# Kernel optimization log

Hardware: AMD Instinct MI355X
Metric: run time of the kernel (lower is better)

## Reference

```python
import jax, jax.numpy as jnp
import numpy as np

B, L, D, NUM_NODES = 256, 512, 128, 1024


def setup_inputs() -> dict:
    key = jax.random.key(0)
    k1, k2, k3, k4, k5, k6 = jax.random.split(key, 6)
    src_ids = jax.random.randint(k1, (B, L), 0, NUM_NODES, dtype=jnp.int32)
    dst_ids = jax.random.randint(k2, (B, L), 0, NUM_NODES, dtype=jnp.int32)
    s = 1.0  # nn.Linear default init is uniform; randn is fine for a numeric baseline
    W1 = jax.random.normal(k3, (1, D), dtype=jnp.float32) * s
    b1 = jax.random.normal(k4, (D,), dtype=jnp.float32) * 0.01
    W2 = jax.random.normal(k5, (D, D), dtype=jnp.float32) * (1.0 / np.sqrt(D))
    b2 = jax.random.normal(k6, (D,), dtype=jnp.float32) * 0.01
    return {"src_ids": src_ids, "dst_ids": dst_ids, "W1": W1, "b1": b1, "W2": W2, "b2": b2}


def _counts_in(a, b):
    # counts_in[i, j] = number of occurrences of a[i, j] within b[i, :]
    # matches np.unique counts / dict-lookup semantics (missing key -> 0)
    return (a[:, :, None] == b[:, None, :]).sum(axis=-1).astype(jnp.float32)


def _encode(appearances, W1, b1, W2, b2):
    # appearances: (B, L, 2) -> unsqueeze(-1) -> Linear(1, D) -> ReLU -> Linear(D, D) -> sum over the 2 count channels
    h = jax.nn.relu(appearances[..., None] * W1[0] + b1)      # (B, L, 2, D)
    h = jnp.einsum('blcd,de->blce', h, W2) + b2               # (B, L, 2, D)
    return h.sum(axis=2)                                      # (B, L, D)


def reference(src_ids, dst_ids, W1, b1, W2, b2):
    # co-occurrence appearance counts
    src_app = jnp.stack([_counts_in(src_ids, src_ids), _counts_in(src_ids, dst_ids)], axis=-1)  # (B, Ls, 2)
    dst_app = jnp.stack([_counts_in(dst_ids, src_ids), _counts_in(dst_ids, dst_ids)], axis=-1)  # (B, Ld, 2)
    # zero out padded positions (node id == 0)
    src_app = jnp.where(src_ids[..., None] == 0, 0.0, src_app)
    dst_app = jnp.where(dst_ids[..., None] == 0, 0.0, dst_app)
    src_feat = _encode(src_app, W1, b1, W2, b2)
    dst_feat = _encode(dst_app, W1, b1, W2, b2)
    return src_feat, dst_feat
```

## Files before the change

kernel.cpp:

```cpp
#include <hip/hip_runtime.h>


#define BB      256
#define LL      512
#define DD      128
#define NNODES  1024
#define CMAX    512
#define SPLITS  4
#define ROWS_PER (LL / SPLITS)

typedef float f4x __attribute__((ext_vector_type(4)));

__global__ __launch_bounds__(DD) void build_table_kernel(
    const float* __restrict__ W1, const float* __restrict__ b1,
    const float* __restrict__ W2, const float* __restrict__ b2,
    float* __restrict__ T) {
  const int c = blockIdx.x;
  const int e = threadIdx.x;
  __shared__ float h[DD];
  h[e] = fmaxf((float)c * W1[e] + b1[e], 0.0f);
  __syncthreads();
  float acc = b2[e];
#pragma unroll 16
  for (int d = 0; d < DD; ++d) acc = fmaf(h[d], W2[d * DD + e], acc);
  T[c * DD + e] = acc;
}

__global__ __launch_bounds__(256) void encode_kernel(
    const int* __restrict__ src_ids, const int* __restrict__ dst_ids,
    const float* __restrict__ T, float* __restrict__ out) {
  const int batch = blockIdx.x >> 2;
  const int split = blockIdx.x & (SPLITS - 1);
  const int tid   = threadIdx.x;

  __shared__ int hist[2 * NNODES];
  __shared__ int cnt[4 * ROWS_PER];

#pragma unroll
  for (int i = tid; i < 2 * NNODES; i += 256) hist[i] = 0;
  __syncthreads();

  const int* sb = src_ids + batch * LL;
  const int* db = dst_ids + batch * LL;
#pragma unroll
  for (int i = tid; i < LL; i += 256) {
    atomicAdd(&hist[sb[i]], 1);
    atomicAdd(&hist[NNODES + db[i]], 1);
  }
  __syncthreads();

  const int r0 = split * ROWS_PER;
  if (tid < ROWS_PER) {
    const int sid = sb[r0 + tid];
    const int did = db[r0 + tid];
    cnt[tid]                = sid ? hist[sid] : 0;
    cnt[ROWS_PER + tid]     = sid ? hist[NNODES + sid] : 0;
    cnt[2 * ROWS_PER + tid] = did ? hist[did] : 0;
    cnt[3 * ROWS_PER + tid] = did ? hist[NNODES + did] : 0;
  }
  __syncthreads();

  const int lane = tid & 31;
  const int rsub = tid >> 5;
  float* out_s = out + ((size_t)batch * LL + r0) * DD;
  float* out_d = out_s + (size_t)BB * LL * DD;

#pragma unroll 4
  for (int rr = rsub; rr < ROWS_PER; rr += 8) {
    const f4x a = ((const f4x*)(T + (size_t)cnt[rr] * DD))[lane];
    const f4x b = ((const f4x*)(T + (size_t)cnt[ROWS_PER + rr] * DD))[lane];
    const f4x c = ((const f4x*)(T + (size_t)cnt[2 * ROWS_PER + rr] * DD))[lane];
    const f4x d = ((const f4x*)(T + (size_t)cnt[3 * ROWS_PER + rr] * DD))[lane];
    const f4x vs = a + b;
    const f4x vd = c + d;
    __builtin_nontemporal_store(vs, ((f4x*)(out_s + (size_t)rr * DD)) + lane);
    __builtin_nontemporal_store(vd, ((f4x*)(out_d + (size_t)rr * DD)) + lane);
  }
}

extern "C" void kernel_launch(void* const* d_in, const int* in_sizes, int n_in,
                              void* d_out, int out_size, void* d_ws, size_t ws_size,
                              hipStream_t stream) {
  const int*   src = (const int*)d_in[0];
  const int*   dst = (const int*)d_in[1];
  const float* W1  = (const float*)d_in[2];
  const float* b1  = (const float*)d_in[3];
  const float* W2  = (const float*)d_in[4];
  const float* b2  = (const float*)d_in[5];
  float* out = (float*)d_out;
  float* T   = (float*)d_ws;

  build_table_kernel<<<CMAX + 1, DD, 0, stream>>>(W1, b1, W2, b2, T);
  encode_kernel<<<BB * SPLITS, 256, 0, stream>>>(src, dst, T, out);
}
```

Before: 157.3 us.

## Move histogram counting into prep kernel and stream encode via packed counts

Histogram and count computation now run in the table-building prep kernel (extra blocks, one per batch), which writes four packed 16-bit counts per position to workspace. The encode kernel becomes a grid-stride gather/store loop over the packed counts, with no shared-memory histogram and no barriers. This removes the histogram that was rebuilt four times per batch and frees the encode blocks from LDS use and syncs. The cost is an extra global round trip for the count array.

```diff
diff --git a/kernel.cpp b/kernel.cpp
--- a/kernel.cpp
+++ b/kernel.cpp
@@ -6,75 +6,77 @@
 #define DD      128
 #define NNODES  1024
 #define CMAX    512
-#define SPLITS  4
-#define ROWS_PER (LL / SPLITS)
+#define TBLOCKS 257
 
 typedef float f4x __attribute__((ext_vector_type(4)));
 
-__global__ __launch_bounds__(DD) void build_table_kernel(
+__global__ __launch_bounds__(256) void prep_kernel(
+    const int* __restrict__ src_ids, const int* __restrict__ dst_ids,
     const float* __restrict__ W1, const float* __restrict__ b1,
     const float* __restrict__ W2, const float* __restrict__ b2,
-    float* __restrict__ T) {
-  const int c = blockIdx.x;
-  const int e = threadIdx.x;
-  __shared__ float h[DD];
-  h[e] = fmaxf((float)c * W1[e] + b1[e], 0.0f);
-  __syncthreads();
-  float acc = b2[e];
+    float* __restrict__ T, uint2* __restrict__ cnt4) {
+  __shared__ int hist[2 * NNODES];
+  const int tid = threadIdx.x;
+
+  if (blockIdx.x < TBLOCKS) {
+    float* h = (float*)hist;
+    const int half = tid >> 7;
+    const int e    = tid & (DD - 1);
+    const int c    = blockIdx.x * 2 + half;
+    const int cc   = (c <= CMAX) ? c : CMAX;
+    h[half * DD + e] = fmaxf((float)cc * W1[e] + b1[e], 0.0f);
+    __syncthreads();
+    float acc = b2[e];
 #pragma unroll 16
-  for (int d = 0; d < DD; ++d) acc = fmaf(h[d], W2[d * DD + e], acc);
-  T[c * DD + e] = acc;
+    for (int d = 0; d < DD; ++d) acc = fmaf(h[half * DD + d], W2[d * DD + e], acc);
+    if (c <= CMAX) T[c * DD + e] = acc;
+  } else {
+    const int batch = blockIdx.x - TBLOCKS;
+#pragma unroll
+    for (int i = tid; i < 2 * NNODES; i += 256) hist[i] = 0;
+    __syncthreads();
+    const int* sb = src_ids + batch * LL;
+    const int* db = dst_ids + batch * LL;
+#pragma unroll
+    for (int i = tid; i < LL; i += 256) {
+      atomicAdd(&hist[sb[i]], 1);
+      atomicAdd(&hist[NNODES + db[i]], 1);
+    }
+    __syncthreads();
+#pragma unroll
+    for (int l = tid; l < LL; l += 256) {
+      const int sid = sb[l];
+      const int did = db[l];
+      const unsigned css = sid ? (unsigned)hist[sid] : 0u;
+      const unsigned csd = sid ? (unsigned)hist[NNODES + sid] : 0u;
+      const unsigned cds = did ? (unsigned)hist[did] : 0u;
+      const unsigned cdd = did ? (unsigned)hist[NNODES + did] : 0u;
+      cnt4[batch * LL + l] = make_uint2(css | (csd << 16), cds | (cdd << 16));
+    }
+  }
 }
 
 __global__ __launch_bounds__(256) void encode_kernel(
-    const int* __restrict__ src_ids, const int* __restrict__ dst_ids,
-    const float* __restrict__ T, float* __restrict__ out) {
-  const int batch = blockIdx.x >> 2;
-  const int split = blockIdx.x & (SPLITS - 1);
-  const int tid   = threadIdx.x;
+    const uint2* __restrict__ cnt4, const float* __restrict__ T,
+    float* __restrict__ out) {
+  const int lane = threadIdx.x & 31;
+  const int rsub = threadIdx.x >> 5;
+  const size_t OUT_OFF = (size_t)BB * LL * DD;
+  const int NGROUPS = (BB * LL) / 8;
 
-  __shared__ int hist[2 * NNODES];
-  __shared__ int cnt[4 * ROWS_PER];
-
-#pragma unroll
-  for (int i = tid; i < 2 * NNODES; i += 256) hist[i] = 0;
-  __syncthreads();
-
-  const int* sb = src_ids + batch * LL;
-  const int* db = dst_ids + batch * LL;
-#pragma unroll
-  for (int i = tid; i < LL; i += 256) {
-    atomicAdd(&hist[sb[i]], 1);
-    atomicAdd(&hist[NNODES + db[i]], 1);
-  }
-  __syncthreads();
-
-  const int r0 = split * ROWS_PER;
-  if (tid < ROWS_PER) {
-    const int sid = sb[r0 + tid];
-    const int did = db[r0 + tid];
-    cnt[tid]                = sid ? hist[sid] : 0;
-    cnt[ROWS_PER + tid]     = sid ? hist[NNODES + sid] : 0;
-    cnt[2 * ROWS_PER + tid] = did ? hist[did] : 0;
-    cnt[3 * ROWS_PER + tid] = did ? hist[NNODES + did] : 0;
-  }
-  __syncthreads();
-
-  const int lane = tid & 31;
-  const int rsub = tid >> 5;
-  float* out_s = out + ((size_t)batch * LL + r0) * DD;
-  float* out_d = out_s + (size_t)BB * LL * DD;
-
-#pragma unroll 4
-  for (int rr = rsub; rr < ROWS_PER; rr += 8) {
-    const f4x a = ((const f4x*)(T + (size_t)cnt[rr] * DD))[lane];
-    const f4x b = ((const f4x*)(T + (size_t)cnt[ROWS_PER + rr] * DD))[lane];
-    const f4x c = ((const f4x*)(T + (size_t)cnt[2 * ROWS_PER + rr] * DD))[lane];
-    const f4x d = ((const f4x*)(T + (size_t)cnt[3 * ROWS_PER + rr] * DD))[lane];
+  for (int g = blockIdx.x; g < NGROUPS; g += gridDim.x) {
+    const int p = g * 8 + rsub;
+    const uint2 c4 = cnt4[p];
+    const int c_ss = c4.x & 0xffff, c_sd = c4.x >> 16;
+    const int c_ds = c4.y & 0xffff, c_dd = c4.y >> 16;
+    const f4x a = ((const f4x*)(T + c_ss * DD))[lane];
+    const f4x b = ((const f4x*)(T + c_sd * DD))[lane];
+    const f4x c = ((const f4x*)(T + c_ds * DD))[lane];
+    const f4x d = ((const f4x*)(T + c_dd * DD))[lane];
     const f4x vs = a + b;
     const f4x vd = c + d;
-    __builtin_nontemporal_store(vs, ((f4x*)(out_s + (size_t)rr * DD)) + lane);
-    __builtin_nontemporal_store(vd, ((f4x*)(out_d + (size_t)rr * DD)) + lane);
+    __builtin_nontemporal_store(vs, ((f4x*)(out + (size_t)p * DD)) + lane);
+    __builtin_nontemporal_store(vd, ((f4x*)(out + OUT_OFF + (size_t)p * DD)) + lane);
   }
 }
 
@@ -87,9 +89,10 @@
   const float* b1  = (const float*)d_in[3];
   const float* W2  = (const float*)d_in[4];
   const float* b2  = (const float*)d_in[5];
-  float* out = (float*)d_out;
-  float* T   = (float*)d_ws;
+  float* out  = (float*)d_out;
+  float* T    = (float*)d_ws;
+  uint2* cnt4 = (uint2*)(T + 66048);
 
-  build_table_kernel<<<CMAX + 1, DD, 0, stream>>>(W1, b1, W2, b2, T);
-  encode_kernel<<<BB * SPLITS, 256, 0, stream>>>(src, dst, T, out);
+  prep_kernel<<<TBLOCKS + BB, 256, 0, stream>>>(src, dst, W1, b1, W2, b2, T, cnt4);
+  encode_kernel<<<2048, 256, 0, stream>>>(cnt4, T, out);
 }
```

Measured after the change: 157.4 us. Within noise of the previous version (+0.0%).
